# Performance work log

Measured on AMD Instinct MI355X. Metric: run time of the kernel, lower is better.

The kernel has to match this reference:

```python
import jax, jax.numpy as jnp
import numpy as np

N = 50000      # nodes
E = 800000     # edges
F_IN = 128     # input feature dim
HID = 64       # hidden_channels
HEADS = 4      # num_heads
HD = HEADS * HID
NS = 0.2       # leaky_relu negative_slope
EPS = 1e-5     # batchnorm eps


def setup_inputs() -> dict:
    key = jax.random.key(0)
    ks = jax.random.split(key, 20)
    rn = lambda k, shp, sc=0.05: jax.random.normal(k, shp, jnp.float32) * sc
    inp = {}
    inp['x'] = jax.random.normal(ks[0], (N, F_IN), jnp.float32)
    inp['edge_index'] = jax.random.randint(ks[1], (2, E), 0, N, dtype=jnp.int32)
    inp['edge_attr'] = jax.random.uniform(ks[2], (E, 1), dtype=jnp.float32)
    # GATConv layer 0: in=F_IN, out=HID per head, concat=True
    inp['W0'] = rn(ks[3], (F_IN, HD)); inp['as0'] = rn(ks[4], (HEADS, HID)); inp['ad0'] = rn(ks[5], (HEADS, HID)); inp['b0'] = jnp.zeros((HD,), jnp.float32)
    # GATConv layer 1: in=HD, concat=True
    inp['W1'] = rn(ks[6], (HD, HD)); inp['as1'] = rn(ks[7], (HEADS, HID)); inp['ad1'] = rn(ks[8], (HEADS, HID)); inp['b1'] = jnp.zeros((HD,), jnp.float32)
    # GATConv layer 2: in=HD, concat=False (heads averaged)
    inp['W2'] = rn(ks[9], (HD, HD)); inp['as2'] = rn(ks[10], (HEADS, HID)); inp['ad2'] = rn(ks[11], (HEADS, HID)); inp['b2'] = jnp.zeros((HID,), jnp.float32)
    # BatchNorm affine params
    inp['g0'] = jnp.ones((HD,), jnp.float32); inp['be0'] = jnp.zeros((HD,), jnp.float32)
    inp['g1'] = jnp.ones((HD,), jnp.float32); inp['be1'] = jnp.zeros((HD,), jnp.float32)
    inp['g2'] = jnp.ones((HID,), jnp.float32); inp['be2'] = jnp.zeros((HID,), jnp.float32)
    # Edge MLP: (3*HID+1) -> 2*HID -> HID -> 1
    inp['Wm1'] = rn(ks[12], (3 * HID + 1, 2 * HID)); inp['bm1'] = jnp.zeros((2 * HID,), jnp.float32)
    inp['Wm2'] = rn(ks[13], (2 * HID, HID)); inp['bm2'] = jnp.zeros((HID,), jnp.float32)
    inp['Wm3'] = rn(ks[14], (HID, 1)); inp['bm3'] = jnp.zeros((1,), jnp.float32)
    return inp


def _gat(x, src, dst, W, a_s, a_d, b, concat):
    """PyG GATConv: gather -> linear -> attention -> segment softmax -> scatter-add.
    Adds self-loops (PyG default)."""
    n = x.shape[0]
    H, D = a_s.shape
    h = (x @ W).reshape(n, H, D)                       # [N, H, D]
    loop = jnp.arange(n, dtype=src.dtype)
    s = jnp.concatenate([src, loop])                   # [E+N]
    d = jnp.concatenate([dst, loop])
    alpha_src = jnp.einsum('nhd,hd->nh', h, a_s)       # [N, H]
    alpha_dst = jnp.einsum('nhd,hd->nh', h, a_d)
    e = jax.nn.leaky_relu(alpha_src[s] + alpha_dst[d], NS)   # [E+N, H]
    # numerically stable segment softmax over incoming edges per dst node
    m = jax.ops.segment_max(e, d, num_segments=n)
    ex = jnp.exp(e - m[d])
    den = jax.ops.segment_sum(ex, d, num_segments=n)
    att = ex / den[d]                                  # [E+N, H]
    out = jax.ops.segment_sum(h[s] * att[:, :, None], d, num_segments=n)  # [N, H, D]
    if concat:
        return out.reshape(n, H * D) + b
    return out.mean(axis=1) + b


def _bn(x, g, b):
    # BatchNorm1d, training-mode statistics (biased variance), deterministic
    mu = x.mean(axis=0)
    var = x.var(axis=0)
    return (x - mu) * jax.lax.rsqrt(var + EPS) * g + b


def reference(x, edge_index, edge_attr,
              W0, as0, ad0, b0, g0, be0,
              W1, as1, ad1, b1, g1, be1,
              W2, as2, ad2, b2, g2, be2,
              Wm1, bm1, Wm2, bm2, Wm3, bm3):
    src, dst = edge_index[0], edge_index[1]
    h = _gat(x, src, dst, W0, as0, ad0, b0, True)
    h = jax.nn.leaky_relu(_bn(h, g0, be0), NS)
    h = _gat(h, src, dst, W1, as1, ad1, b1, True)
    h = jax.nn.leaky_relu(_bn(h, g1, be1), NS)
    h = _gat(h, src, dst, W2, as2, ad2, b2, False)
    h = _bn(h, g2, be2)                                # [N, HID]
    hs, hd = h[src], h[dst]                            # gathers: [E, HID]
    ef = jnp.concatenate([hs, hd, jnp.abs(hs - hd), edge_attr], axis=1)  # [E, 3*HID+1]
    ef = jax.nn.leaky_relu(ef @ Wm1 + bm1, NS)
    ef = jax.nn.leaky_relu(ef @ Wm2 + bm2, NS)
    return (ef @ Wm3 + bm3).squeeze(-1)                # [E] edge logits
```

## Files before the change

### kernel.cpp

```cpp
#include <hip/hip_runtime.h>
#include <math.h>

#define Nn 50000
#define Npad 50048
#define Ee 800000
#define FIN 128
#define HIDd 64
#define NH 4
#define HD 256
#define NEG 0.2f
#define BEPS 1e-5f

typedef __attribute__((ext_vector_type(8))) short short8;
typedef __attribute__((ext_vector_type(4))) float f32x4;
typedef unsigned int uint;
typedef unsigned short ushort;

static __device__ __forceinline__ float lrelu(float x) { return x > 0.f ? x : NEG * x; }
static __device__ __forceinline__ float bf2f(ushort x) {
  return __uint_as_float(((uint)x) << 16);
}
static __device__ __forceinline__ ushort f2bf(float f) {
  uint u = __float_as_uint(f);
  return (ushort)((u + 0x7FFF + ((u >> 16) & 1)) >> 16);
}

__global__ void fill_kernel(float* __restrict__ p, float v, int n) {
  int i = blockIdx.x * 256 + threadIdx.x;
  if (i < n) p[i] = v;
}

__global__ void filli_kernel(int* __restrict__ p, int v, int n) {
  int i = blockIdx.x * 256 + threadIdx.x;
  if (i < n) p[i] = v;
}

__global__ void hist_kernel(const int* __restrict__ dst, int* __restrict__ deg) {
  int i = blockIdx.x * 256 + threadIdx.x;
  if (i < Ee) atomicAdd(&deg[dst[i]], 1);
}

__global__ __launch_bounds__(1024) void scan_kernel(const int* __restrict__ deg,
                                                    int* __restrict__ rowstart) {
  __shared__ int ts[1024];
  const int tid = threadIdx.x;
  const int CH = (Nn + 1023) / 1024;
  const int base = tid * CH;
  int s = 0;
  for (int j = 0; j < CH; j++) {
    int idx = base + j;
    if (idx < Nn) s += deg[idx];
  }
  ts[tid] = s;
  __syncthreads();
  for (int off = 1; off < 1024; off <<= 1) {
    int v = (tid >= off) ? ts[tid - off] : 0;
    __syncthreads();
    ts[tid] += v;
    __syncthreads();
  }
  int run = (tid == 0) ? 0 : ts[tid - 1];
  for (int j = 0; j < CH; j++) {
    int idx = base + j;
    if (idx < Nn) {
      rowstart[idx] = run;
      run += deg[idx];
      if (idx == Nn - 1) rowstart[Nn] = run;
    }
  }
}

__global__ void cursor_init_kernel(const int* __restrict__ rowstart, int* __restrict__ cursor) {
  int i = blockIdx.x * 256 + threadIdx.x;
  if (i < Nn) cursor[i] = rowstart[i];
}

__global__ void elist_fill_kernel(const int* __restrict__ src, const int* __restrict__ dst,
                                  int* __restrict__ cursor, int* __restrict__ elist) {
  int i = blockIdx.x * 256 + threadIdx.x;
  if (i >= Ee + Nn) return;
  int s, d;
  if (i < Ee) { s = src[i]; d = dst[i]; } else { s = d = i - Ee; }
  int pos = atomicAdd(&cursor[d], 1);
  elist[pos] = s;
}

__global__ void cvt_bf16_kernel(const float* __restrict__ in, ushort* __restrict__ out, int n) {
  int i = blockIdx.x * 256 + threadIdx.x;
  if (i < n) out[i] = f2bf(in[i]);
}

__global__ void wfrag_kernel(const float* __restrict__ W, ushort* __restrict__ Wf, int K) {
  int idx = blockIdx.x * 256 + threadIdx.x;
  int total = (K >> 5) * 16 * 64 * 8;
  if (idx >= total) return;
  int j = idx & 7, lane = (idx >> 3) & 63, t = (idx >> 9) & 15, kc = idx >> 13;
  int n = t * 16 + (lane & 15);
  int k = kc * 32 + ((lane >> 4) << 3) + j;
  Wf[idx] = f2bf(W[k * 256 + n]);
}

__global__ __launch_bounds__(256) void gemm_mfma_kernel(
    const ushort* __restrict__ A, const ushort* __restrict__ Bf, ushort* __restrict__ C, int K,
    const float* __restrict__ a_s, const float* __restrict__ a_d,
    float* __restrict__ asrc, float* __restrict__ adst) {
  const int tid = threadIdx.x;
  const int w = tid >> 6, lane = tid & 63;
  const int q = lane >> 4, nn = lane & 15;
  const int m0 = blockIdx.x * 128 + w * 32;
  const int cb = blockIdx.y;
  f32x4 acc[2][8];
#pragma unroll
  for (int tm = 0; tm < 2; tm++)
#pragma unroll
    for (int t = 0; t < 8; t++) acc[tm][t] = (f32x4){0.f, 0.f, 0.f, 0.f};
  const int nkc = K >> 5;
  for (int kc = 0; kc < nkc; kc++) {
    short8 a0 = *(const short8*)(A + (size_t)(m0 + nn) * K + kc * 32 + q * 8);
    short8 a1 = *(const short8*)(A + (size_t)(m0 + 16 + nn) * K + kc * 32 + q * 8);
#pragma unroll
    for (int t = 0; t < 8; t++) {
      short8 b = *(const short8*)(Bf + ((size_t)((kc * 16 + cb * 8 + t) * 64 + lane)) * 8);
      acc[0][t] = __builtin_amdgcn_mfma_f32_16x16x32_bf16(a0, b, acc[0][t], 0, 0, 0);
      acc[1][t] = __builtin_amdgcn_mfma_f32_16x16x32_bf16(a1, b, acc[1][t], 0, 0, 0);
    }
  }
  float asv[8], adv[8];
#pragma unroll
  for (int t = 0; t < 8; t++) {
    int head = 2 * cb + (t >> 2);
    int dim = (t & 3) * 16 + nn;
    asv[t] = a_s[head * 64 + dim];
    adv[t] = a_d[head * 64 + dim];
  }
#pragma unroll
  for (int tm = 0; tm < 2; tm++) {
    float ps[2][4] = {{0.f, 0.f, 0.f, 0.f}, {0.f, 0.f, 0.f, 0.f}};
    float pd[2][4] = {{0.f, 0.f, 0.f, 0.f}, {0.f, 0.f, 0.f, 0.f}};
#pragma unroll
    for (int t = 0; t < 8; t++) {
      int hp = t >> 2;
#pragma unroll
      for (int r = 0; r < 4; r++) {
        float v = acc[tm][t][r];
        int row = m0 + tm * 16 + q * 4 + r;
        C[(size_t)row * 256 + cb * 128 + t * 16 + nn] = f2bf(v);
        ps[hp][r] = fmaf(v, asv[t], ps[hp][r]);
        pd[hp][r] = fmaf(v, adv[t], pd[hp][r]);
      }
    }
#pragma unroll
    for (int hp = 0; hp < 2; hp++)
#pragma unroll
      for (int r = 0; r < 4; r++) {
        float s = ps[hp][r], d2 = pd[hp][r];
        s += __shfl_xor(s, 1); s += __shfl_xor(s, 2);
        s += __shfl_xor(s, 4); s += __shfl_xor(s, 8);
        d2 += __shfl_xor(d2, 1); d2 += __shfl_xor(d2, 2);
        d2 += __shfl_xor(d2, 4); d2 += __shfl_xor(d2, 8);
        if (nn == 0) {
          int row = m0 + tm * 16 + q * 4 + r;
          asrc[row * 4 + 2 * cb + hp] = s;
          adst[row * 4 + 2 * cb + hp] = d2;
        }
      }
  }
}

__global__ __launch_bounds__(256) void gat_gather_kernel(
    const int* __restrict__ elist, const int* __restrict__ rowstart,
    const ushort* __restrict__ h, const float* __restrict__ asrc,
    const float* __restrict__ adst, const float* __restrict__ bias,
    float* __restrict__ agg, int concat) {
  __shared__ float accs[4][256];
  __shared__ float dens[4][4];
  const int n = blockIdx.x;
  const int tid = threadIdx.x;
  const int w = tid >> 6, lane = tid & 63;
  const int hh = lane >> 4;
  const int start = rowstart[n], end = rowstart[n + 1];
  const float adstv = adst[n * 4 + hh];
  float4 acc = make_float4(0.f, 0.f, 0.f, 0.f);
  float den = 0.f;
  int j = start + w;
  for (; j + 12 < end; j += 16) {
    int s0 = elist[j], s1 = elist[j + 4], s2 = elist[j + 8], s3 = elist[j + 12];
    float e0 = asrc[s0 * 4 + hh] + adstv;
    float e1 = asrc[s1 * 4 + hh] + adstv;
    float e2 = asrc[s2 * 4 + hh] + adstv;
    float e3 = asrc[s3 * 4 + hh] + adstv;
    ushort4 v0 = *(const ushort4*)(h + (size_t)s0 * HD + lane * 4);
    ushort4 v1 = *(const ushort4*)(h + (size_t)s1 * HD + lane * 4);
    ushort4 v2 = *(const ushort4*)(h + (size_t)s2 * HD + lane * 4);
    ushort4 v3 = *(const ushort4*)(h + (size_t)s3 * HD + lane * 4);
    float w0 = __expf(lrelu(e0)), w1 = __expf(lrelu(e1));
    float w2 = __expf(lrelu(e2)), w3 = __expf(lrelu(e3));
    den += (w0 + w1) + (w2 + w3);
    acc.x = fmaf(w0, bf2f(v0.x), acc.x); acc.y = fmaf(w0, bf2f(v0.y), acc.y);
    acc.z = fmaf(w0, bf2f(v0.z), acc.z); acc.w = fmaf(w0, bf2f(v0.w), acc.w);
    acc.x = fmaf(w1, bf2f(v1.x), acc.x); acc.y = fmaf(w1, bf2f(v1.y), acc.y);
    acc.z = fmaf(w1, bf2f(v1.z), acc.z); acc.w = fmaf(w1, bf2f(v1.w), acc.w);
    acc.x = fmaf(w2, bf2f(v2.x), acc.x); acc.y = fmaf(w2, bf2f(v2.y), acc.y);
    acc.z = fmaf(w2, bf2f(v2.z), acc.z); acc.w = fmaf(w2, bf2f(v2.w), acc.w);
    acc.x = fmaf(w3, bf2f(v3.x), acc.x); acc.y = fmaf(w3, bf2f(v3.y), acc.y);
    acc.z = fmaf(w3, bf2f(v3.z), acc.z); acc.w = fmaf(w3, bf2f(v3.w), acc.w);
  }
  for (; j < end; j += 4) {
    int s0 = elist[j];
    float e0 = asrc[s0 * 4 + hh] + adstv;
    ushort4 v0 = *(const ushort4*)(h + (size_t)s0 * HD + lane * 4);
    float w0 = __expf(lrelu(e0));
    den += w0;
    acc.x = fmaf(w0, bf2f(v0.x), acc.x); acc.y = fmaf(w0, bf2f(v0.y), acc.y);
    acc.z = fmaf(w0, bf2f(v0.z), acc.z); acc.w = fmaf(w0, bf2f(v0.w), acc.w);
  }
  *(float4*)&accs[w][lane * 4] = acc;
  if ((lane & 15) == 0) dens[w][hh] = den;
  __syncthreads();
  const int d = tid;
  float s = (accs[0][d] + accs[1][d]) + (accs[2][d] + accs[3][d]);
  const int hd = d >> 6;
  float dn = (dens[0][hd] + dens[1][hd]) + (dens[2][hd] + dens[3][hd]);
  float o = s / dn;
  if (concat) o += bias[d];
  agg[(size_t)n * HD + d] = o;
}

__global__ void mean_heads_kernel(const float* __restrict__ agg, const float* __restrict__ b,
                                  float* __restrict__ h2) {
  int i = blockIdx.x * 256 + threadIdx.x;
  if (i >= Nn * HIDd) return;
  int n = i >> 6, dd = i & 63;
  const float* r = agg + (size_t)n * HD + dd;
  h2[i] = 0.25f * (r[0] + r[64] + r[128] + r[192]) + b[dd];
}

__global__ void bn_stats_kernel(const float* __restrict__ x, float* __restrict__ stats,
                                int nrows, int C) {
  int r0 = blockIdx.x * 512;
  int tpc = 256 / C;
  int c = threadIdx.x % C;
  int ro = threadIdx.x / C;
  int rend = min(r0 + 512, nrows);
  float s = 0.f, s2 = 0.f;
  for (int r = r0 + ro; r < rend; r += tpc) {
    float v = x[(size_t)r * C + c];
    s += v; s2 += v * v;
  }
  atomicAdd(&stats[c], s);
  atomicAdd(&stats[C + c], s2);
}

__global__ void bn_apply_bf16_kernel(const float* __restrict__ x, const float* __restrict__ stats,
                                     const float* __restrict__ g, const float* __restrict__ be,
                                     ushort* __restrict__ outb, int C, int do_lrelu) {
  int i = blockIdx.x * 256 + threadIdx.x;
  if (i >= Nn * C) return;
  int c = i % C;
  float mu = stats[c] * (1.f / Nn);
  float var = stats[C + c] * (1.f / Nn) - mu * mu;
  float y = (x[i] - mu) * rsqrtf(var + BEPS) * g[c] + be[c];
  if (do_lrelu) y = lrelu(y);
  outb[i] = f2bf(y);
}

__global__ void w1frag_kernel(const float* __restrict__ Wm1, ushort* __restrict__ W1f) {
  int idx = blockIdx.x * 256 + threadIdx.x;
  if (idx >= 7 * 8 * 64 * 8) return;
  int j = idx & 7, lane = (idx >> 3) & 63, tile = (idx >> 9) & 7, chunk = idx >> 12;
  int n = tile * 16 + (lane & 15);
  int k = chunk * 32 + (lane >> 4) * 8 + j;
  W1f[idx] = (k < 193) ? f2bf(Wm1[k * 128 + n]) : (ushort)0;
}

__global__ void w2frag_kernel(const float* __restrict__ Wm2, ushort* __restrict__ W2f) {
  int idx = blockIdx.x * 256 + threadIdx.x;
  if (idx >= 4 * 4 * 64 * 8) return;
  int j = idx & 7, lane = (idx >> 3) & 63, tile = (idx >> 9) & 3, chunk = idx >> 11;
  int n = tile * 16 + (lane & 15);
  int k = chunk * 32 + (lane >> 4) * 8 + j;
  W2f[idx] = f2bf(Wm2[k * 64 + n]);
}

static __device__ __forceinline__ short8 absdiff8(short8 a, short8 b) {
  short8 r;
#pragma unroll
  for (int j = 0; j < 8; j++) r[j] = (short)f2bf(fabsf(bf2f((ushort)a[j]) - bf2f((ushort)b[j])));
  return r;
}

#define MLP1_STEP(c, e0x, e1x)                                                         \
  {                                                                                    \
    short8 _a0 = (e0x);                                                                \
    short8 _a1 = (e1x);                                                                \
    const uint4* bp = (const uint4*)W1f + (c) * 512 + lane;                            \
    _Pragma("unroll") for (int t = 0; t < 8; t++) {                                    \
      uint4 braw = bp[t * 64];                                                         \
      short8 b = *(short8*)&braw;                                                      \
      acc0[t] = __builtin_amdgcn_mfma_f32_16x16x32_bf16(_a0, b, acc0[t], 0, 0, 0);     \
      acc1[t] = __builtin_amdgcn_mfma_f32_16x16x32_bf16(_a1, b, acc1[t], 0, 0, 0);     \
    }                                                                                  \
  }

__global__ __launch_bounds__(256) void edge_mlp_mfma_kernel(
    const ushort* __restrict__ hb, const int* __restrict__ src, const int* __restrict__ dst,
    const float* __restrict__ eattr, const ushort* __restrict__ W1f,
    const ushort* __restrict__ W2f, const float* __restrict__ bm1,
    const float* __restrict__ bm2, const float* __restrict__ Wm3,
    const float* __restrict__ bm3, float* __restrict__ out) {
  __shared__ ushort t1s[4][16 * 136];
  const int tid = threadIdx.x;
  const int w = tid >> 6, lane = tid & 63;
  const int q = lane >> 4, nn = lane & 15;

  float bm1v[8];
#pragma unroll
  for (int t = 0; t < 8; t++) bm1v[t] = bm1[t * 16 + nn];
  float bm2v[4], w3v[4];
#pragma unroll
  for (int t = 0; t < 4; t++) { bm2v[t] = bm2[t * 16 + nn]; w3v[t] = Wm3[t * 16 + nn]; }
  const float bm3v = bm3[0];

  const int base = blockIdx.x * 128 + w * 32;
  const int e0 = base + nn, e1 = base + 16 + nn;
  const int s0 = src[e0], d0 = dst[e0];
  const int s1 = src[e1], d1 = dst[e1];
  const float at0 = eattr[e0], at1 = eattr[e1];

  short8 hs0a = *(const short8*)(hb + s0 * 64 + q * 8);
  short8 hs0b = *(const short8*)(hb + s0 * 64 + 32 + q * 8);
  short8 hd0a = *(const short8*)(hb + d0 * 64 + q * 8);
  short8 hd0b = *(const short8*)(hb + d0 * 64 + 32 + q * 8);
  short8 hs1a = *(const short8*)(hb + s1 * 64 + q * 8);
  short8 hs1b = *(const short8*)(hb + s1 * 64 + 32 + q * 8);
  short8 hd1a = *(const short8*)(hb + d1 * 64 + q * 8);
  short8 hd1b = *(const short8*)(hb + d1 * 64 + 32 + q * 8);

  f32x4 acc0[8], acc1[8];
#pragma unroll
  for (int t = 0; t < 8; t++) {
    acc0[t] = (f32x4){0.f, 0.f, 0.f, 0.f};
    acc1[t] = (f32x4){0.f, 0.f, 0.f, 0.f};
  }

  short8 a6_0 = 0, a6_1 = 0;
  if (q == 0) { a6_0[0] = (short)f2bf(at0); a6_1[0] = (short)f2bf(at1); }

  MLP1_STEP(0, hs0a, hs1a)
  MLP1_STEP(1, hs0b, hs1b)
  MLP1_STEP(2, hd0a, hd1a)
  MLP1_STEP(3, hd0b, hd1b)
  MLP1_STEP(4, absdiff8(hs0a, hd0a), absdiff8(hs1a, hd1a))
  MLP1_STEP(5, absdiff8(hs0b, hd0b), absdiff8(hs1b, hd1b))
  MLP1_STEP(6, a6_0, a6_1)

  ushort* myt1 = t1s[w];
  auto do_group = [&](f32x4* acc, int g) {
#pragma unroll
    for (int t = 0; t < 8; t++)
#pragma unroll
      for (int r = 0; r < 4; r++)
        myt1[(q * 4 + r) * 136 + t * 16 + nn] = f2bf(lrelu(acc[t][r] + bm1v[t]));
    f32x4 acc2[4];
#pragma unroll
    for (int t = 0; t < 4; t++) acc2[t] = (f32x4){0.f, 0.f, 0.f, 0.f};
#pragma unroll
    for (int c2 = 0; c2 < 4; c2++) {
      short8 a = *(short8*)&myt1[nn * 136 + c2 * 32 + q * 8];
#pragma unroll
      for (int t = 0; t < 4; t++) {
        short8 b = *(const short8*)(W2f + ((size_t)(c2 * 4 + t) * 64 + lane) * 8);
        acc2[t] = __builtin_amdgcn_mfma_f32_16x16x32_bf16(a, b, acc2[t], 0, 0, 0);
      }
    }
#pragma unroll
    for (int r = 0; r < 4; r++) {
      float sum = 0.f;
#pragma unroll
      for (int t = 0; t < 4; t++) sum += lrelu(acc2[t][r] + bm2v[t]) * w3v[t];
      sum += __shfl_xor(sum, 1);
      sum += __shfl_xor(sum, 2);
      sum += __shfl_xor(sum, 4);
      sum += __shfl_xor(sum, 8);
      if (nn == 0) out[base + g * 16 + q * 4 + r] = sum + bm3v;
    }
  };
  do_group(acc0, 0);
  do_group(acc1, 1);
}

extern "C" void kernel_launch(void* const* d_in, const int* in_sizes, int n_in,
                              void* d_out, int out_size, void* d_ws, size_t ws_size,
                              hipStream_t stream) {
  const float* x    = (const float*)d_in[0];
  const int*   ei   = (const int*)d_in[1];
  const float* eatt = (const float*)d_in[2];
  const float* W0 = (const float*)d_in[3];
  const float* as0 = (const float*)d_in[4];
  const float* ad0 = (const float*)d_in[5];
  const float* b0 = (const float*)d_in[6];
  const float* W1 = (const float*)d_in[7];
  const float* as1 = (const float*)d_in[8];
  const float* ad1 = (const float*)d_in[9];
  const float* b1 = (const float*)d_in[10];
  const float* W2 = (const float*)d_in[11];
  const float* as2 = (const float*)d_in[12];
  const float* ad2 = (const float*)d_in[13];
  const float* b2 = (const float*)d_in[14];
  const float* g0 = (const float*)d_in[15];
  const float* be0 = (const float*)d_in[16];
  const float* g1 = (const float*)d_in[17];
  const float* be1 = (const float*)d_in[18];
  const float* g2 = (const float*)d_in[19];
  const float* be2 = (const float*)d_in[20];
  const float* Wm1 = (const float*)d_in[21];
  const float* bm1 = (const float*)d_in[22];
  const float* Wm2 = (const float*)d_in[23];
  const float* bm2 = (const float*)d_in[24];
  const float* Wm3 = (const float*)d_in[25];
  const float* bm3 = (const float*)d_in[26];
  const int* src = ei;
  const int* dst = ei + Ee;
  float* out = (float*)d_out;

  char* w = (char*)d_ws;
  float*  agg  = (float*)w;
  ushort* xb   = (ushort*)w;
  ushort* hB   = (ushort*)(w + (size_t)Npad * 256 * 4);
  float*  h2   = (float*)hB;
  ushort* aggb = (ushort*)(w + (size_t)Npad * 256 * 6);
  ushort* hb2  = aggb;
  float*  asrc = (float*)(w + (size_t)Npad * 256 * 8);
  float*  adst = asrc + (size_t)Npad * 4;
  float*  stats = adst + (size_t)Npad * 4;
  int* deg      = (int*)(stats + 512);
  int* rowstart = deg + Nn;
  int* cursor   = rowstart + Nn + 16;
  int* elist    = cursor + Nn;
  ushort* W0f  = (ushort*)(elist + Ee + Nn);
  ushort* W1gf = W0f + 32768;
  ushort* W2gf = W1gf + 65536;
  ushort* eW1f = W2gf + 65536;
  ushort* eW2f = eW1f + 28672;

  filli_kernel<<<(Nn + 255) / 256, 256, 0, stream>>>(deg, 1, Nn);
  hist_kernel<<<(Ee + 255) / 256, 256, 0, stream>>>(dst, deg);
  scan_kernel<<<1, 1024, 0, stream>>>(deg, rowstart);
  cursor_init_kernel<<<(Nn + 255) / 256, 256, 0, stream>>>(rowstart, cursor);
  elist_fill_kernel<<<(Ee + Nn + 255) / 256, 256, 0, stream>>>(src, dst, cursor, elist);

  wfrag_kernel<<<(32768 + 255) / 256, 256, 0, stream>>>(W0, W0f, FIN);
  wfrag_kernel<<<(65536 + 255) / 256, 256, 0, stream>>>(W1, W1gf, HD);
  wfrag_kernel<<<(65536 + 255) / 256, 256, 0, stream>>>(W2, W2gf, HD);
  w1frag_kernel<<<(7 * 8 * 64 * 8 + 255) / 256, 256, 0, stream>>>(Wm1, eW1f);
  w2frag_kernel<<<(4 * 4 * 64 * 8 + 255) / 256, 256, 0, stream>>>(Wm2, eW2f);

  auto gat = [&](const ushort* Ab, const ushort* Wf, int K, const float* a_s,
                 const float* a_d, const float* bias, bool concat) {
    gemm_mfma_kernel<<<dim3(Npad / 128, 2), 256, 0, stream>>>(Ab, Wf, hB, K, a_s, a_d,
                                                              asrc, adst);
    gat_gather_kernel<<<Nn, 256, 0, stream>>>(elist, rowstart, hB, asrc, adst, bias, agg,
                                              concat ? 1 : 0);
  };

  cvt_bf16_kernel<<<(Nn * FIN + 255) / 256, 256, 0, stream>>>(x, xb, Nn * FIN);
  gat(xb, W0f, FIN, as0, ad0, b0, true);
  fill_kernel<<<2, 256, 0, stream>>>(stats, 0.f, 512);
  bn_stats_kernel<<<(Nn + 511) / 512, 256, 0, stream>>>(agg, stats, Nn, HD);
  bn_apply_bf16_kernel<<<(Nn * HD + 255) / 256, 256, 0, stream>>>(agg, stats, g0, be0, aggb, HD, 1);
  gat(aggb, W1gf, HD, as1, ad1, b1, true);
  fill_kernel<<<2, 256, 0, stream>>>(stats, 0.f, 512);
  bn_stats_kernel<<<(Nn + 511) / 512, 256, 0, stream>>>(agg, stats, Nn, HD);
  bn_apply_bf16_kernel<<<(Nn * HD + 255) / 256, 256, 0, stream>>>(agg, stats, g1, be1, aggb, HD, 1);
  gat(aggb, W2gf, HD, as2, ad2, b2, false);
  mean_heads_kernel<<<(Nn * HIDd + 255) / 256, 256, 0, stream>>>(agg, b2, h2);
  fill_kernel<<<1, 256, 0, stream>>>(stats, 0.f, 128);
  bn_stats_kernel<<<(Nn + 511) / 512, 256, 0, stream>>>(h2, stats, Nn, HIDd);
  bn_apply_bf16_kernel<<<(Nn * HIDd + 255) / 256, 256, 0, stream>>>(h2, stats, g2, be2, hb2,
                                                                    HIDd, 0);
  edge_mlp_mfma_kernel<<<Ee / 128, 256, 0, stream>>>(hb2, src, dst, eatt, eW1f, eW2f, bm1, bm2,
                                                     Wm3, bm3, out);
}
```

Baseline: 1.152 ms.

## Store GAT features head-major and split gather per head with bf16 aggregation

The GEMM now writes projected features in a head-major layout ([head][node][64]), and the gather kernel launches one 64-thread block per (node, head). Each lane reads one bf16 element per neighbor, which removes the shared-memory reduction and block sync. For concat layers the gather writes bf16 output directly. BatchNorm stats and apply then run on that bf16 buffer in place instead of on an fp32 intermediate, cutting memory traffic. In exchange, neighbor reads become 128-byte rows per head with more, smaller blocks. Pre-BN values are also rounded to bf16, which can reduce accuracy.

```diff
diff --git a/kernel.cpp b/kernel.cpp
--- a/kernel.cpp
+++ b/kernel.cpp
@@ -101,7 +101,7 @@
 }
 
 __global__ __launch_bounds__(256) void gemm_mfma_kernel(
-    const ushort* __restrict__ A, const ushort* __restrict__ Bf, ushort* __restrict__ C, int K,
+    const ushort* __restrict__ A, const ushort* __restrict__ Bf, ushort* __restrict__ Chm, int K,
     const float* __restrict__ a_s, const float* __restrict__ a_d,
     float* __restrict__ asrc, float* __restrict__ adst) {
   const int tid = threadIdx.x;
@@ -140,11 +140,13 @@
 #pragma unroll
     for (int t = 0; t < 8; t++) {
       int hp = t >> 2;
+      int head = 2 * cb + hp;
+      int dim = (t & 3) * 16 + nn;
 #pragma unroll
       for (int r = 0; r < 4; r++) {
         float v = acc[tm][t][r];
         int row = m0 + tm * 16 + q * 4 + r;
-        C[(size_t)row * 256 + cb * 128 + t * 16 + nn] = f2bf(v);
+        Chm[((size_t)head * Npad + row) * 64 + dim] = f2bf(v);
         ps[hp][r] = fmaf(v, asv[t], ps[hp][r]);
         pd[hp][r] = fmaf(v, adv[t], pd[hp][r]);
       }
@@ -167,63 +169,52 @@
   }
 }
 
-__global__ __launch_bounds__(256) void gat_gather_kernel(
+__global__ __launch_bounds__(64) void gat_gather_kernel(
     const int* __restrict__ elist, const int* __restrict__ rowstart,
     const ushort* __restrict__ h, const float* __restrict__ asrc,
     const float* __restrict__ adst, const float* __restrict__ bias,
-    float* __restrict__ agg, int concat) {
-  __shared__ float accs[4][256];
-  __shared__ float dens[4][4];
+    ushort* __restrict__ aggb, float* __restrict__ aggf, int concat) {
   const int n = blockIdx.x;
-  const int tid = threadIdx.x;
-  const int w = tid >> 6, lane = tid & 63;
-  const int hh = lane >> 4;
+  const int hh = blockIdx.y;
+  const int lane = threadIdx.x;
   const int start = rowstart[n], end = rowstart[n + 1];
   const float adstv = adst[n * 4 + hh];
-  float4 acc = make_float4(0.f, 0.f, 0.f, 0.f);
-  float den = 0.f;
-  int j = start + w;
-  for (; j + 12 < end; j += 16) {
-    int s0 = elist[j], s1 = elist[j + 4], s2 = elist[j + 8], s3 = elist[j + 12];
+  const ushort* hbase = h + ((size_t)hh * Npad) * 64 + lane;
+  float acc = 0.f, den = 0.f;
+  int j = start;
+  for (; j + 3 < end; j += 4) {
+    int s0 = elist[j], s1 = elist[j + 1], s2 = elist[j + 2], s3 = elist[j + 3];
     float e0 = asrc[s0 * 4 + hh] + adstv;
     float e1 = asrc[s1 * 4 + hh] + adstv;
     float e2 = asrc[s2 * 4 + hh] + adstv;
     float e3 = asrc[s3 * 4 + hh] + adstv;
-    ushort4 v0 = *(const ushort4*)(h + (size_t)s0 * HD + lane * 4);
-    ushort4 v1 = *(const ushort4*)(h + (size_t)s1 * HD + lane * 4);
-    ushort4 v2 = *(const ushort4*)(h + (size_t)s2 * HD + lane * 4);
-    ushort4 v3 = *(const ushort4*)(h + (size_t)s3 * HD + lane * 4);
+    ushort v0 = hbase[(size_t)s0 * 64];
+    ushort v1 = hbase[(size_t)s1 * 64];
+    ushort v2 = hbase[(size_t)s2 * 64];
+    ushort v3 = hbase[(size_t)s3 * 64];
     float w0 = __expf(lrelu(e0)), w1 = __expf(lrelu(e1));
     float w2 = __expf(lrelu(e2)), w3 = __expf(lrelu(e3));
     den += (w0 + w1) + (w2 + w3);
-    acc.x = fmaf(w0, bf2f(v0.x), acc.x); acc.y = fmaf(w0, bf2f(v0.y), acc.y);
-    acc.z = fmaf(w0, bf2f(v0.z), acc.z); acc.w = fmaf(w0, bf2f(v0.w), acc.w);
-    acc.x = fmaf(w1, bf2f(v1.x), acc.x); acc.y = fmaf(w1, bf2f(v1.y), acc.y);
-    acc.z = fmaf(w1, bf2f(v1.z), acc.z); acc.w = fmaf(w1, bf2f(v1.w), acc.w);
-    acc.x = fmaf(w2, bf2f(v2.x), acc.x); acc.y = fmaf(w2, bf2f(v2.y), acc.y);
-    acc.z = fmaf(w2, bf2f(v2.z), acc.z); acc.w = fmaf(w2, bf2f(v2.w), acc.w);
-    acc.x = fmaf(w3, bf2f(v3.x), acc.x); acc.y = fmaf(w3, bf2f(v3.y), acc.y);
-    acc.z = fmaf(w3, bf2f(v3.z), acc.z); acc.w = fmaf(w3, bf2f(v3.w), acc.w);
-  }
-  for (; j < end; j += 4) {
+    acc = fmaf(w0, bf2f(v0), acc);
+    acc = fmaf(w1, bf2f(v1), acc);
+    acc = fmaf(w2, bf2f(v2), acc);
+    acc = fmaf(w3, bf2f(v3), acc);
+  }
+  for (; j < end; j++) {
     int s0 = elist[j];
     float e0 = asrc[s0 * 4 + hh] + adstv;
-    ushort4 v0 = *(const ushort4*)(h + (size_t)s0 * HD + lane * 4);
+    ushort v0 = hbase[(size_t)s0 * 64];
     float w0 = __expf(lrelu(e0));
     den += w0;
-    acc.x = fmaf(w0, bf2f(v0.x), acc.x); acc.y = fmaf(w0, bf2f(v0.y), acc.y);
-    acc.z = fmaf(w0, bf2f(v0.z), acc.z); acc.w = fmaf(w0, bf2f(v0.w), acc.w);
-  }
-  *(float4*)&accs[w][lane * 4] = acc;
-  if ((lane & 15) == 0) dens[w][hh] = den;
-  __syncthreads();
-  const int d = tid;
-  float s = (accs[0][d] + accs[1][d]) + (accs[2][d] + accs[3][d]);
-  const int hd = d >> 6;
-  float dn = (dens[0][hd] + dens[1][hd]) + (dens[2][hd] + dens[3][hd]);
-  float o = s / dn;
-  if (concat) o += bias[d];
-  agg[(size_t)n * HD + d] = o;
+    acc = fmaf(w0, bf2f(v0), acc);
+  }
+  float o = acc / den;
+  const int col = hh * 64 + lane;
+  if (concat) {
+    aggb[(size_t)n * HD + col] = f2bf(o + bias[col]);
+  } else {
+    aggf[(size_t)n * HD + col] = o;
+  }
 }
 
 __global__ void mean_heads_kernel(const float* __restrict__ agg, const float* __restrict__ b,
@@ -233,6 +224,22 @@
   int n = i >> 6, dd = i & 63;
   const float* r = agg + (size_t)n * HD + dd;
   h2[i] = 0.25f * (r[0] + r[64] + r[128] + r[192]) + b[dd];
+}
+
+__global__ void bn_stats_bf16_kernel(const ushort* __restrict__ x, float* __restrict__ stats,
+                                     int nrows, int C) {
+  int r0 = blockIdx.x * 512;
+  int tpc = 256 / C;
+  int c = threadIdx.x % C;
+  int ro = threadIdx.x / C;
+  int rend = min(r0 + 512, nrows);
+  float s = 0.f, s2 = 0.f;
+  for (int r = r0 + ro; r < rend; r += tpc) {
+    float v = bf2f(x[(size_t)r * C + c]);
+    s += v; s2 += v * v;
+  }
+  atomicAdd(&stats[c], s);
+  atomicAdd(&stats[C + c], s2);
 }
 
 __global__ void bn_stats_kernel(const float* __restrict__ x, float* __restrict__ stats,
@@ -251,16 +258,27 @@
   atomicAdd(&stats[C + c], s2);
 }
 
+__global__ void bn_apply_inplace_kernel(ushort* __restrict__ x, const float* __restrict__ stats,
+                                        const float* __restrict__ g, const float* __restrict__ be,
+                                        int C) {
+  int i = blockIdx.x * 256 + threadIdx.x;
+  if (i >= Nn * C) return;
+  int c = i % C;
+  float mu = stats[c] * (1.f / Nn);
+  float var = stats[C + c] * (1.f / Nn) - mu * mu;
+  float y = (bf2f(x[i]) - mu) * rsqrtf(var + BEPS) * g[c] + be[c];
+  x[i] = f2bf(lrelu(y));
+}
+
 __global__ void bn_apply_bf16_kernel(const float* __restrict__ x, const float* __restrict__ stats,
                                      const float* __restrict__ g, const float* __restrict__ be,
-                                     ushort* __restrict__ outb, int C, int do_lrelu) {
+                                     ushort* __restrict__ outb, int C) {
   int i = blockIdx.x * 256 + threadIdx.x;
   if (i >= Nn * C) return;
   int c = i % C;
   float mu = stats[c] * (1.f / Nn);
   float var = stats[C + c] * (1.f / Nn) - mu * mu;
   float y = (x[i] - mu) * rsqrtf(var + BEPS) * g[c] + be[c];
-  if (do_lrelu) y = lrelu(y);
   outb[i] = f2bf(y);
 }
 
@@ -459,25 +477,25 @@
                  const float* a_d, const float* bias, bool concat) {
     gemm_mfma_kernel<<<dim3(Npad / 128, 2), 256, 0, stream>>>(Ab, Wf, hB, K, a_s, a_d,
                                                               asrc, adst);
-    gat_gather_kernel<<<Nn, 256, 0, stream>>>(elist, rowstart, hB, asrc, adst, bias, agg,
-                                              concat ? 1 : 0);
+    gat_gather_kernel<<<dim3(Nn, NH), 64, 0, stream>>>(elist, rowstart, hB, asrc, adst, bias,
+                                                       aggb, agg, concat ? 1 : 0);
   };
 
   cvt_bf16_kernel<<<(Nn * FIN + 255) / 256, 256, 0, stream>>>(x, xb, Nn * FIN);
   gat(xb, W0f, FIN, as0, ad0, b0, true);
   fill_kernel<<<2, 256, 0, stream>>>(stats, 0.f, 512);
-  bn_stats_kernel<<<(Nn + 511) / 512, 256, 0, stream>>>(agg, stats, Nn, HD);
-  bn_apply_bf16_kernel<<<(Nn * HD + 255) / 256, 256, 0, stream>>>(agg, stats, g0, be0, aggb, HD, 1);
+  bn_stats_bf16_kernel<<<(Nn + 511) / 512, 256, 0, stream>>>(aggb, stats, Nn, HD);
+  bn_apply_inplace_kernel<<<(Nn * HD + 255) / 256, 256, 0, stream>>>(aggb, stats, g0, be0, HD);
   gat(aggb, W1gf, HD, as1, ad1, b1, true);
   fill_kernel<<<2, 256, 0, stream>>>(stats, 0.f, 512);
-  bn_stats_kernel<<<(Nn + 511) / 512, 256, 0, stream>>>(agg, stats, Nn, HD);
-  bn_apply_bf16_kernel<<<(Nn * HD + 255) / 256, 256, 0, stream>>>(agg, stats, g1, be1, aggb, HD, 1);
+  bn_stats_bf16_kernel<<<(Nn + 511) / 512, 256, 0, stream>>>(aggb, stats, Nn, HD);
+  bn_apply_inplace_kernel<<<(Nn * HD + 255) / 256, 256, 0, stream>>>(aggb, stats, g1, be1, HD);
   gat(aggb, W2gf, HD, as2, ad2, b2, false);
   mean_heads_kernel<<<(Nn * HIDd + 255) / 256, 256, 0, stream>>>(agg, b2, h2);
   fill_kernel<<<1, 256, 0, stream>>>(stats, 0.f, 128);
   bn_stats_kernel<<<(Nn + 511) / 512, 256, 0, stream>>>(h2, stats, Nn, HIDd);
   bn_apply_bf16_kernel<<<(Nn * HIDd + 255) / 256, 256, 0, stream>>>(h2, stats, g2, be2, hb2,
-                                                                    HIDd, 0);
+                                                                    HIDd);
   edge_mlp_mfma_kernel<<<Ee / 128, 256, 0, stream>>>(hb2, src, dst, eatt, eW1f, eW2f, bm1, bm2,
                                                      Wm3, bm3, out);
 }
```

Measured after the change: 1.298 ms. 12.7% more time.
